# Optimization experiments

Measured on AMD Instinct MI355X. Metric: run time of the kernel, lower is better.

Reference implementation:

```python
import jax, jax.numpy as jnp
import numpy as np

N_NODES = 100000


def gcn_layer(x, W, b, src, dst, n):
    # PyG GCNConv: h = x @ W; add self loops; norm = d^-1/2[src]*d^-1/2[dst];
    # out = scatter_add(norm * h[src] -> dst) + b
    h = x @ W  # [N, F_out]
    # append self loops
    loop = jnp.arange(n, dtype=src.dtype)
    s = jnp.concatenate([src, loop])
    d = jnp.concatenate([dst, loop])
    deg = jax.ops.segment_sum(jnp.ones_like(d, dtype=h.dtype), d, num_segments=n)
    dinv = jnp.where(deg > 0, jax.lax.rsqrt(deg), 0.0)
    norm = dinv[s] * dinv[d]  # [E+N]
    msg = h[s] * norm[:, None]  # gather + scale
    out = jax.ops.segment_sum(msg, d, num_segments=n)  # scatter-add
    return out + b


def setup_inputs() -> dict:
    key = jax.random.key(0)
    k1, k2, k3, k4 = jax.random.split(key, 4)
    din, dh = 64, 64
    x = jax.random.normal(k1, (N_NODES, din), dtype=jnp.float32)
    edge_index = jax.random.randint(k2, (2, 1600000), 0, N_NODES, dtype=jnp.int64)
    s1 = 1.0 / np.sqrt(din)
    s2 = 1.0 / np.sqrt(dh)
    W1 = jax.random.uniform(k3, (din, dh), dtype=jnp.float32, minval=-s1, maxval=s1)
    W2 = jax.random.uniform(k4, (dh, dh), dtype=jnp.float32, minval=-s2, maxval=s2)
    b1 = jnp.zeros((dh,), dtype=jnp.float32)
    b2 = jnp.zeros((dh,), dtype=jnp.float32)
    return {"x": x, "edge_index": edge_index, "W1": W1, "b1": b1, "W2": W2, "b2": b2}


def reference(x, edge_index, W1, b1, W2, b2):
    src, dst = edge_index[0], edge_index[1]
    n = x.shape[0]
    h = jax.nn.relu(gcn_layer(x, W1, b1, src, dst, n))
    h = jax.nn.relu(gcn_layer(h, W2, b2, src, dst, n))
    return h
```

## Files before the change

### kernel.cpp

```cpp
#include <hip/hip_runtime.h>
#include <hip/hip_bf16.h>

using bf16s = __hip_bfloat16;
typedef __bf16 bf16x8 __attribute__((ext_vector_type(8)));
typedef float f32x4 __attribute__((ext_vector_type(4)));

constexpr int MS_TILE = 2048;
constexpr int SLAB_CAP = 5120;

__global__ __launch_bounds__(256) void multisplit(const int* __restrict__ src,
                                                  const int* __restrict__ dst,
                                                  int* __restrict__ gcur,
                                                  int* __restrict__ part, int E) {
    __shared__ int cnt[512];
    __shared__ int off[512];
    __shared__ int gbase[512];
    __shared__ int img[MS_TILE];
    __shared__ int tgt[MS_TILE];
    int tid = threadIdx.x;
    for (int tbase = blockIdx.x * MS_TILE; tbase < E; tbase += gridDim.x * MS_TILE) {
        int m = min(MS_TILE, E - tbase);
        for (int i = tid; i < 512; i += 256) cnt[i] = 0;
        __syncthreads();
        int pk[8], bk[8], rk[8];
        int nloc = 0;
        int j0 = tid * 8;
        if (j0 + 8 <= m) {
            int4 s0 = *(const int4*)(src + tbase + j0);
            int4 s1 = *(const int4*)(src + tbase + j0 + 4);
            int4 d0 = *(const int4*)(dst + tbase + j0);
            int4 d1 = *(const int4*)(dst + tbase + j0 + 4);
            int ss[8] = {s0.x, s0.y, s0.z, s0.w, s1.x, s1.y, s1.z, s1.w};
            int dd[8] = {d0.x, d0.y, d0.z, d0.w, d1.x, d1.y, d1.z, d1.w};
#pragma unroll
            for (int k = 0; k < 8; k++) {
                int b = dd[k] >> 8;
                pk[k] = (ss[k] << 8) | (dd[k] & 255);
                bk[k] = b;
                rk[k] = atomicAdd(&cnt[b], 1);
            }
            nloc = 8;
        } else {
            for (int j = j0; j < m; j++) {
                int s = src[tbase + j], d = dst[tbase + j];
                int b = d >> 8;
                pk[nloc] = (s << 8) | (d & 255);
                bk[nloc] = b;
                rk[nloc] = atomicAdd(&cnt[b], 1);
                nloc++;
            }
        }
        __syncthreads();
        if (tid < 64) {
            int base = tid * 8;
            int vals[8];
            int s0 = 0;
#pragma unroll
            for (int j = 0; j < 8; j++) { vals[j] = cnt[base + j]; s0 += vals[j]; }
            int sc = s0;
#pragma unroll
            for (int o = 1; o < 64; o <<= 1) {
                int u = __shfl_up(sc, o);
                if (tid >= o) sc += u;
            }
            int ex = sc - s0;
#pragma unroll
            for (int j = 0; j < 8; j++) { off[base + j] = ex; ex += vals[j]; }
        }
        __syncthreads();
        for (int b = tid; b < 512; b += 256) {
            int c = cnt[b];
            gbase[b] = c ? (b * SLAB_CAP + atomicAdd(&gcur[b], c)) : 0;
        }
        __syncthreads();
        for (int i = 0; i < nloc; i++) {
            int p = off[bk[i]] + rk[i];
            img[p] = pk[i];
            tgt[p] = gbase[bk[i]] + rk[i];
        }
        __syncthreads();
        for (int j = tid; j < m; j += 256) part[tgt[j]] = img[j];
        __syncthreads();
    }
}

__global__ __launch_bounds__(512) void scan_bases(const int* __restrict__ gcur,
                                                  int* __restrict__ bases, int m) {
    __shared__ int lds[512];
    int tid = threadIdx.x;
    int v = (tid < m) ? gcur[tid] : 0;
    lds[tid] = v;
    __syncthreads();
    for (int off = 1; off < 512; off <<= 1) {
        int x = (tid >= off) ? lds[tid - off] : 0;
        __syncthreads();
        lds[tid] += x;
        __syncthreads();
    }
    if (tid <= m) bases[tid] = lds[tid] - v;
}

__global__ __launch_bounds__(256) void bucket_place(const int* __restrict__ gcur,
                                                    const int* __restrict__ bases,
                                                    const int* __restrict__ part,
                                                    int* __restrict__ rowptr,
                                                    int* __restrict__ csr,
                                                    float* __restrict__ dinv, int n) {
    __shared__ int cnt[256];
    __shared__ int cur[256];
    __shared__ int lds[256];
    __shared__ int img[SLAB_CAP];
    int b = blockIdx.x;
    int tid = threadIdx.x;
    int node0 = b << 8;
    int m = gcur[b];
    if (m > SLAB_CAP) m = SLAB_CAP;
    int base = bases[b];
    const int* slab = part + b * SLAB_CAP;
    cnt[tid] = 0;
    __syncthreads();
    for (int j = tid; j < m; j += 256) atomicAdd(&cnt[slab[j] & 255], 1);
    __syncthreads();
    int v = cnt[tid];
    lds[tid] = v;
    __syncthreads();
    for (int off = 1; off < 256; off <<= 1) {
        int x = (tid >= off) ? lds[tid - off] : 0;
        __syncthreads();
        lds[tid] += x;
        __syncthreads();
    }
    int ex = lds[tid] - v;
    cur[tid] = ex;
    int node = node0 + tid;
    if (node <= n) rowptr[node] = base + ex;
    if (node < n) dinv[node] = rsqrtf((float)(v + 1));
    __syncthreads();
    for (int j = tid; j < m; j += 256) {
        int pkv = slab[j];
        int p = atomicAdd(&cur[pkv & 255], 1);
        img[p] = (pkv >> 8) << 5;
    }
    __syncthreads();
    for (int j = tid; j < m; j += 256) csr[base + j] = img[j];
}

template <bool AF32>
__global__ __launch_bounds__(256) void gemm64(const void* __restrict__ A_,
                                              const float* __restrict__ W,
                                              const float* __restrict__ dinv,
                                              bf16s* __restrict__ out, int nrows) {
    int lane = threadIdx.x & 63;
    int wid = (blockIdx.x * blockDim.x + threadIdx.x) >> 6;
    int nwaves = (gridDim.x * blockDim.x) >> 6;
    int r = lane & 15;
    int q = lane >> 4;
    int kb = q * 8;

    bf16x8 bfrag[4][2];
#pragma unroll
    for (int t = 0; t < 4; t++) {
#pragma unroll
        for (int h = 0; h < 2; h++) {
            bf16x8 bb;
            int ncol = t * 16 + r;
            int k0 = h * 32 + kb;
#pragma unroll
            for (int j = 0; j < 8; j++) bb[j] = (__bf16)W[(k0 + j) * 64 + ncol];
            bfrag[t][h] = bb;
        }
    }

    int ntiles = nrows >> 4;
    for (int tile = wid; tile < ntiles; tile += nwaves) {
        bf16x8 a0, a1;
        if (AF32) {
            const float* ap = (const float*)A_ + (size_t)(tile * 16 + r) * 64 + kb;
            f32x4 v0 = *reinterpret_cast<const f32x4*>(ap);
            f32x4 v1 = *reinterpret_cast<const f32x4*>(ap + 4);
            f32x4 v2 = *reinterpret_cast<const f32x4*>(ap + 32);
            f32x4 v3 = *reinterpret_cast<const f32x4*>(ap + 36);
#pragma unroll
            for (int j = 0; j < 4; j++) {
                a0[j] = (__bf16)v0[j]; a0[4 + j] = (__bf16)v1[j];
                a1[j] = (__bf16)v2[j]; a1[4 + j] = (__bf16)v3[j];
            }
        } else {
            const __bf16* ap = (const __bf16*)A_ + (size_t)(tile * 16 + r) * 64 + kb;
            a0 = *reinterpret_cast<const bf16x8*>(ap);
            a1 = *reinterpret_cast<const bf16x8*>(ap + 32);
        }
        f32x4 c[4];
#pragma unroll
        for (int t = 0; t < 4; t++) {
            f32x4 acc = {0.f, 0.f, 0.f, 0.f};
            acc = __builtin_amdgcn_mfma_f32_16x16x32_bf16(a0, bfrag[t][0], acc, 0, 0, 0);
            acc = __builtin_amdgcn_mfma_f32_16x16x32_bf16(a1, bfrag[t][1], acc, 0, 0, 0);
            c[t] = acc;
        }
        float dr[4];
#pragma unroll
        for (int g = 0; g < 4; g++) dr[g] = dinv[tile * 16 + q * 4 + g];
#pragma unroll
        for (int t = 0; t < 4; t++) {
#pragma unroll
            for (int g = 0; g < 4; g++) {
                int row = tile * 16 + q * 4 + g;
                out[(size_t)row * 64 + t * 16 + r] = __float2bfloat16(c[t][g] * dr[g]);
            }
        }
    }
}

template <bool OUTF32>
__global__ __launch_bounds__(256) void aggregate(const bf16s* __restrict__ t,
                                                 const float* __restrict__ dinv,
                                                 const int* __restrict__ rowptr,
                                                 const int* __restrict__ csr,
                                                 const float* __restrict__ bias,
                                                 void* __restrict__ out_, int n) {
    int gid = blockIdx.x * blockDim.x + threadIdx.x;
    int v = gid >> 6;
    if (v >= n) return;
    int lane = gid & 63;
    int half = lane >> 5;
    int c = lane & 31;
    const unsigned* trow = (const unsigned*)t;
    unsigned sw = trow[(size_t)v * 32 + c];
    float ax, ay;
    if (half == 0) {
        ax = __uint_as_float(sw << 16);
        ay = __uint_as_float(sw & 0xffff0000u);
    } else {
        ax = 0.f; ay = 0.f;
    }
    int beg = rowptr[v], end = rowptr[v + 1];
    for (int j = beg; j < end; j += 16) {
        int idx[8];
        float wgt[8];
#pragma unroll
        for (int k = 0; k < 8; k++) {
            int jj = j + 2 * k + half;
            bool ok = jj < end;
            idx[k] = csr[ok ? jj : beg];
            wgt[k] = ok ? 1.f : 0.f;
        }
        unsigned w[8];
#pragma unroll
        for (int k = 0; k < 8; k++) w[k] = trow[idx[k] + c];
#pragma unroll
        for (int k = 0; k < 8; k++) {
            ax = fmaf(wgt[k], __uint_as_float(w[k] << 16), ax);
            ay = fmaf(wgt[k], __uint_as_float(w[k] & 0xffff0000u), ay);
        }
    }
    ax += __shfl_xor(ax, 32);
    ay += __shfl_xor(ay, 32);
    if (half == 0) {
        float dv = dinv[v];
        float2 bb = ((const float2*)bias)[c];
        float ox = fmaxf(fmaf(dv, ax, bb.x), 0.f);
        float oy = fmaxf(fmaf(dv, ay, bb.y), 0.f);
        if (OUTF32) {
            float2 o2; o2.x = ox; o2.y = oy;
            ((float2*)out_)[(size_t)v * 32 + c] = o2;
        } else {
            unsigned ua = __float_as_uint(ox);
            unsigned ub = __float_as_uint(oy);
            ua = (ua + 0x7fffu + ((ua >> 16) & 1u)) >> 16;
            ub = (ub + 0x7fffu + ((ub >> 16) & 1u));
            ((unsigned*)out_)[(size_t)v * 32 + c] = (ua & 0xffffu) | (ub & 0xffff0000u);
        }
    }
}

extern "C" void kernel_launch(void* const* d_in, const int* in_sizes, int n_in,
                              void* d_out, int out_size, void* d_ws, size_t ws_size,
                              hipStream_t stream) {
    const float* x  = (const float*)d_in[0];
    const int*   ei = (const int*)d_in[1];
    const float* W1 = (const float*)d_in[2];
    const float* b1 = (const float*)d_in[3];
    const float* W2 = (const float*)d_in[4];
    const float* b2 = (const float*)d_in[5];
    float* out = (float*)d_out;

    int n = in_sizes[0] / 64;
    int E = in_sizes[1] / 2;
    const int* src = ei;
    const int* dst = ei + E;
    int nbuck = (n + 255) >> 8;

    char* w = (char*)d_ws;
    auto alloc = [&](size_t bytes) -> void* {
        void* p = (void*)w;
        w += (bytes + 255) & ~(size_t)255;
        return p;
    };
    int*   gcur   = (int*)alloc(2048);
    int*   bases  = (int*)alloc(2048);
    int*   rowptr = (int*)alloc((size_t)(n + 1) * 4);
    int*   csr    = (int*)alloc((size_t)E * 4);
    float* dinv   = (float*)alloc((size_t)n * 4);
    size_t slab_bytes = (size_t)nbuck * SLAB_CAP * 4;
    size_t tbuf_bytes = (size_t)n * 64 * 2;
    char*  ovl    = (char*)alloc(slab_bytes > tbuf_bytes ? slab_bytes : tbuf_bytes);
    int*   part   = (int*)ovl;
    bf16s* tbuf   = (bf16s*)ovl;
    bf16s* h1     = (bf16s*)alloc((size_t)n * 64 * 2);

    hipMemsetAsync(gcur, 0, 2048, stream);

    int ntiles = (E + MS_TILE - 1) / MS_TILE;
    multisplit<<<ntiles, 256, 0, stream>>>(src, dst, gcur, part, E);
    scan_bases<<<1, 512, 0, stream>>>(gcur, bases, nbuck);
    bucket_place<<<nbuck, 256, 0, stream>>>(gcur, bases, part, rowptr, csr, dinv, n);

    gemm64<true><<<256, 256, 0, stream>>>(x, W1, dinv, tbuf, n);
    aggregate<false><<<(n * 64 + 255) / 256, 256, 0, stream>>>(tbuf, dinv, rowptr, csr, b1, h1, n);
    gemm64<false><<<256, 256, 0, stream>>>(h1, W2, dinv, tbuf, n);
    aggregate<true><<<(n * 64 + 255) / 256, 256, 0, stream>>>(tbuf, dinv, rowptr, csr, b2, out, n);
}
```

Measured before the change: 232.0 us.

## Pad CSR rows to multiples of 8 with sentinel zero row, drop scan kernel

Builds a per-bucket fixed-capacity CSR whose rows are padded to multiples of 8 with a sentinel index pointing at an appended zero row, so the aggregate loop needs no bounds checks or weights and can load indices as int4 vectors. The global scan_bases kernel is removed since each bucket writes at a fixed offset, and per-node (offset, padded degree) pairs replace rowptr. Aggregation now uses 32 lanes per node instead of a split 64-lane wave with a shuffle reduction. The padding adds extra gathers of the zero row and more CSR memory, and overflow handling clamps slab positions.

```diff
diff --git a/kernel.cpp b/kernel.cpp
--- a/kernel.cpp
+++ b/kernel.cpp
@@ -7,6 +7,16 @@
 
 constexpr int MS_TILE = 2048;
 constexpr int SLAB_CAP = 5120;
+constexpr int CSR_CAP = 7168;
+
+__device__ inline float uasf(unsigned u) { return __uint_as_float(u); }
+
+__device__ inline unsigned pk2(float x, float y) {
+    unsigned ux = __float_as_uint(x), uy = __float_as_uint(y);
+    ux = (ux + 0x7fffu + ((ux >> 16) & 1u)) >> 16;
+    uy = (uy + 0x7fffu + ((uy >> 16) & 1u)) & 0xffff0000u;
+    return (ux & 0xffffu) | uy;
+}
 
 __global__ __launch_bounds__(256) void multisplit(const int* __restrict__ src,
                                                   const int* __restrict__ dst,
@@ -70,7 +80,11 @@
         __syncthreads();
         for (int b = tid; b < 512; b += 256) {
             int c = cnt[b];
-            gbase[b] = c ? (b * SLAB_CAP + atomicAdd(&gcur[b], c)) : 0;
+            if (c) {
+                int st = atomicAdd(&gcur[b], c);
+                if (st > SLAB_CAP - c) st = SLAB_CAP - c;
+                gbase[b] = b * SLAB_CAP + st;
+            }
         }
         __syncthreads();
         for (int i = 0; i < nloc; i++) {
@@ -84,45 +98,27 @@
     }
 }
 
-__global__ __launch_bounds__(512) void scan_bases(const int* __restrict__ gcur,
-                                                  int* __restrict__ bases, int m) {
-    __shared__ int lds[512];
-    int tid = threadIdx.x;
-    int v = (tid < m) ? gcur[tid] : 0;
-    lds[tid] = v;
-    __syncthreads();
-    for (int off = 1; off < 512; off <<= 1) {
-        int x = (tid >= off) ? lds[tid - off] : 0;
-        __syncthreads();
-        lds[tid] += x;
-        __syncthreads();
-    }
-    if (tid <= m) bases[tid] = lds[tid] - v;
-}
-
 __global__ __launch_bounds__(256) void bucket_place(const int* __restrict__ gcur,
-                                                    const int* __restrict__ bases,
                                                     const int* __restrict__ part,
-                                                    int* __restrict__ rowptr,
+                                                    int2* __restrict__ rinfo,
                                                     int* __restrict__ csr,
                                                     float* __restrict__ dinv, int n) {
     __shared__ int cnt[256];
     __shared__ int cur[256];
     __shared__ int lds[256];
-    __shared__ int img[SLAB_CAP];
+    __shared__ int img[CSR_CAP];
     int b = blockIdx.x;
     int tid = threadIdx.x;
     int node0 = b << 8;
-    int m = gcur[b];
-    if (m > SLAB_CAP) m = SLAB_CAP;
-    int base = bases[b];
+    int m = min(gcur[b], SLAB_CAP);
     const int* slab = part + b * SLAB_CAP;
     cnt[tid] = 0;
     __syncthreads();
     for (int j = tid; j < m; j += 256) atomicAdd(&cnt[slab[j] & 255], 1);
     __syncthreads();
-    int v = cnt[tid];
-    lds[tid] = v;
+    int deg = cnt[tid];
+    int pdeg = (deg + 7) & ~7;
+    lds[tid] = pdeg;
     __syncthreads();
     for (int off = 1; off < 256; off <<= 1) {
         int x = (tid >= off) ? lds[tid - off] : 0;
@@ -130,11 +126,17 @@
         lds[tid] += x;
         __syncthreads();
     }
-    int ex = lds[tid] - v;
+    int ex = lds[tid] - pdeg;
     cur[tid] = ex;
+    int mpad = lds[255];
     int node = node0 + tid;
-    if (node <= n) rowptr[node] = base + ex;
-    if (node < n) dinv[node] = rsqrtf((float)(v + 1));
+    if (node < n) {
+        rinfo[node] = make_int2(b * CSR_CAP + ex, pdeg);
+        dinv[node] = rsqrtf((float)(deg + 1));
+    }
+    __syncthreads();
+    int sent = n << 5;
+    for (int j = tid; j < mpad; j += 256) img[j] = sent;
     __syncthreads();
     for (int j = tid; j < m; j += 256) {
         int pkv = slab[j];
@@ -142,7 +144,8 @@
         img[p] = (pkv >> 8) << 5;
     }
     __syncthreads();
-    for (int j = tid; j < m; j += 256) csr[base + j] = img[j];
+    int* dp = csr + b * CSR_CAP;
+    for (int j = tid; j < mpad; j += 256) dp[j] = img[j];
 }
 
 template <bool AF32>
@@ -157,6 +160,8 @@
     int q = lane >> 4;
     int kb = q * 8;
 
+    if (wid == 0) out[(size_t)nrows * 64 + lane] = __float2bfloat16(0.f);
+
     bf16x8 bfrag[4][2];
 #pragma unroll
     for (int t = 0; t < 4; t++) {
@@ -213,64 +218,43 @@
 }
 
 template <bool OUTF32>
-__global__ __launch_bounds__(256) void aggregate(const bf16s* __restrict__ t,
+__global__ __launch_bounds__(256) void aggregate(const unsigned* __restrict__ t32,
                                                  const float* __restrict__ dinv,
-                                                 const int* __restrict__ rowptr,
+                                                 const int2* __restrict__ rinfo,
                                                  const int* __restrict__ csr,
                                                  const float* __restrict__ bias,
                                                  void* __restrict__ out_, int n) {
     int gid = blockIdx.x * blockDim.x + threadIdx.x;
-    int v = gid >> 6;
+    int v = gid >> 5;
     if (v >= n) return;
-    int lane = gid & 63;
-    int half = lane >> 5;
-    int c = lane & 31;
-    const unsigned* trow = (const unsigned*)t;
-    unsigned sw = trow[(size_t)v * 32 + c];
-    float ax, ay;
-    if (half == 0) {
-        ax = __uint_as_float(sw << 16);
-        ay = __uint_as_float(sw & 0xffff0000u);
+    int c = gid & 31;
+    int2 ri = rinfo[v];
+    unsigned sw = t32[(size_t)v * 32 + c];
+    float ax = uasf(sw << 16);
+    float ay = uasf(sw & 0xffff0000u);
+    const int* cp = csr + ri.x;
+    for (int j = 0; j < ri.y; j += 8) {
+        int4 e0 = *(const int4*)(cp + j);
+        int4 e1 = *(const int4*)(cp + j + 4);
+        int idx[8] = {e0.x, e0.y, e0.z, e0.w, e1.x, e1.y, e1.z, e1.w};
+        unsigned g[8];
+#pragma unroll
+        for (int k = 0; k < 8; k++) g[k] = t32[(size_t)idx[k] + c];
+#pragma unroll
+        for (int k = 0; k < 8; k++) {
+            ax += uasf(g[k] << 16);
+            ay += uasf(g[k] & 0xffff0000u);
+        }
+    }
+    float dv = dinv[v];
+    float2 bb = ((const float2*)bias)[c];
+    float ox = fmaxf(fmaf(dv, ax, bb.x), 0.f);
+    float oy = fmaxf(fmaf(dv, ay, bb.y), 0.f);
+    if (OUTF32) {
+        float2 o2; o2.x = ox; o2.y = oy;
+        ((float2*)out_)[(size_t)v * 32 + c] = o2;
     } else {
-        ax = 0.f; ay = 0.f;
-    }
-    int beg = rowptr[v], end = rowptr[v + 1];
-    for (int j = beg; j < end; j += 16) {
-        int idx[8];
-        float wgt[8];
-#pragma unroll
-        for (int k = 0; k < 8; k++) {
-            int jj = j + 2 * k + half;
-            bool ok = jj < end;
-            idx[k] = csr[ok ? jj : beg];
-            wgt[k] = ok ? 1.f : 0.f;
-        }
-        unsigned w[8];
-#pragma unroll
-        for (int k = 0; k < 8; k++) w[k] = trow[idx[k] + c];
-#pragma unroll
-        for (int k = 0; k < 8; k++) {
-            ax = fmaf(wgt[k], __uint_as_float(w[k] << 16), ax);
-            ay = fmaf(wgt[k], __uint_as_float(w[k] & 0xffff0000u), ay);
-        }
-    }
-    ax += __shfl_xor(ax, 32);
-    ay += __shfl_xor(ay, 32);
-    if (half == 0) {
-        float dv = dinv[v];
-        float2 bb = ((const float2*)bias)[c];
-        float ox = fmaxf(fmaf(dv, ax, bb.x), 0.f);
-        float oy = fmaxf(fmaf(dv, ay, bb.y), 0.f);
-        if (OUTF32) {
-            float2 o2; o2.x = ox; o2.y = oy;
-            ((float2*)out_)[(size_t)v * 32 + c] = o2;
-        } else {
-            unsigned ua = __float_as_uint(ox);
-            unsigned ub = __float_as_uint(oy);
-            ua = (ua + 0x7fffu + ((ua >> 16) & 1u)) >> 16;
-            ub = (ub + 0x7fffu + ((ub >> 16) & 1u));
-            ((unsigned*)out_)[(size_t)v * 32 + c] = (ua & 0xffffu) | (ub & 0xffff0000u);
-        }
+        ((unsigned*)out_)[(size_t)v * 32 + c] = pk2(ox, oy);
     }
 }
 
@@ -298,26 +282,25 @@
         return p;
     };
     int*   gcur   = (int*)alloc(2048);
-    int*   bases  = (int*)alloc(2048);
-    int*   rowptr = (int*)alloc((size_t)(n + 1) * 4);
-    int*   csr    = (int*)alloc((size_t)E * 4);
+    int2*  rinfo  = (int2*)alloc((size_t)n * 8);
+    int*   csr    = (int*)alloc((size_t)nbuck * CSR_CAP * 4);
     float* dinv   = (float*)alloc((size_t)n * 4);
     size_t slab_bytes = (size_t)nbuck * SLAB_CAP * 4;
-    size_t tbuf_bytes = (size_t)n * 64 * 2;
+    size_t tbuf_bytes = (size_t)(n + 16) * 64 * 2;
     char*  ovl    = (char*)alloc(slab_bytes > tbuf_bytes ? slab_bytes : tbuf_bytes);
     int*   part   = (int*)ovl;
     bf16s* tbuf   = (bf16s*)ovl;
-    bf16s* h1     = (bf16s*)alloc((size_t)n * 64 * 2);
+    bf16s* h1     = (bf16s*)alloc((size_t)(n + 16) * 64 * 2);
 
     hipMemsetAsync(gcur, 0, 2048, stream);
 
     int ntiles = (E + MS_TILE - 1) / MS_TILE;
     multisplit<<<ntiles, 256, 0, stream>>>(src, dst, gcur, part, E);
-    scan_bases<<<1, 512, 0, stream>>>(gcur, bases, nbuck);
-    bucket_place<<<nbuck, 256, 0, stream>>>(gcur, bases, part, rowptr, csr, dinv, n);
-
+    bucket_place<<<nbuck, 256, 0, stream>>>(gcur, part, rinfo, csr, dinv, n);
+
+    int agrid = (n * 32 + 255) / 256;
     gemm64<true><<<256, 256, 0, stream>>>(x, W1, dinv, tbuf, n);
-    aggregate<false><<<(n * 64 + 255) / 256, 256, 0, stream>>>(tbuf, dinv, rowptr, csr, b1, h1, n);
+    aggregate<false><<<agrid, 256, 0, stream>>>((const unsigned*)tbuf, dinv, rinfo, csr, b1, h1, n);
     gemm64<false><<<256, 256, 0, stream>>>(h1, W2, dinv, tbuf, n);
-    aggregate<true><<<(n * 64 + 255) / 256, 256, 0, stream>>>(tbuf, dinv, rowptr, csr, b2, out, n);
-}
+    aggregate<true><<<agrid, 256, 0, stream>>>((const unsigned*)tbuf, dinv, rinfo, csr, b2, out, n);
+}
```

New measurement: 205.4 us. 11.5% less time.
